# Kernel optimization log

Hardware: AMD Instinct MI355X
Metric: run time of the kernel (lower is better)

The kernel has to match this reference:

```python
import jax, jax.numpy as jnp
import numpy as np

NEG_INF = -1000000000.0

N, T, D, H = 2, 4096, 512, 8
S = D // H  # size_per_head = 64


def setup_inputs() -> dict:
    key = jax.random.key(0)
    ks = jax.random.split(key, 6)
    scale = 1.0 / np.sqrt(D)
    return {
        "query": jax.random.normal(ks[0], (N, T, D), dtype=jnp.float32),
        "reference": jax.random.normal(ks[1], (N, T, D), dtype=jnp.float32),
        "padding_mask": jnp.zeros((N, 1, 1, T), dtype=jnp.float32),
        "Wq": jax.random.normal(ks[2], (D, H, S), dtype=jnp.float32) * scale,
        "Wk": jax.random.normal(ks[3], (D, H, S), dtype=jnp.float32) * scale,
        "Wv": jax.random.normal(ks[4], (D, H, S), dtype=jnp.float32) * scale,
        "Wo": jax.random.normal(ks[5], (H, S, D), dtype=jnp.float32) * scale,
    }


def reference(query, reference, padding_mask, Wq, Wk, Wv, Wo):
    # split projections: [N,T,D] x [D,H,S] -> [N,T,H,S]
    q = jnp.einsum("NTD,DHS->NTHS", query, Wq) * (S ** -0.5)
    k = jnp.einsum("NTD,DHS->NTHS", reference, Wk)
    v = jnp.einsum("NTD,DHS->NTHS", reference, Wv)
    # scores [N,H,Q,R]; mask is 0/1, scaled by NEG_INF (as in source)
    scores = jnp.einsum("NQHS,NRHS->NHQR", q, k) + padding_mask * NEG_INF
    probs = jax.nn.softmax(scores, axis=3)
    # dropout is identity (training=False)
    ctx = jnp.einsum("NHQR,NRHS->NQHS", probs, v)
    # merge projection: [N,Q,H,S] x [H,S,D] -> [N,Q,D]
    return jnp.einsum("NTHS,HSD->NTD", ctx, Wo)
```

## Files before the change

### kernel.cpp

```cpp
#include <hip/hip_runtime.h>
#include <stdint.h>

using u16    = unsigned short;
using u32    = unsigned int;
using short8 = __attribute__((ext_vector_type(8))) short;
using s16x4  = __attribute__((ext_vector_type(4))) short;
using f32x4  = __attribute__((ext_vector_type(4))) float;
using f32x16 = __attribute__((ext_vector_type(16))) float;
using i32x4  = __attribute__((ext_vector_type(4))) int;

constexpr float LOG2E = 1.44269504088896340736f;


__device__ __forceinline__ u16 f2bf(float f) {
  uint32_t u = __builtin_bit_cast(uint32_t, f);
  return (u16)((u + 0x7fffu + ((u >> 16) & 1u)) >> 16);
}

__device__ __forceinline__ void gload16(const void* g, void* l) {
  __builtin_amdgcn_global_load_lds(
      (const __attribute__((address_space(1))) unsigned int*)g,
      (__attribute__((address_space(3))) unsigned int*)l, 16, 0, 0);
}

__device__ __forceinline__ u32 cvtpk_bf16(float lo, float hi) {
  u32 r;
  asm("v_cvt_pk_bf16_f32 %0, %1, %2" : "=v"(r) : "v"(lo), "v"(hi));
  return r;
}

__device__ __forceinline__ f32x16 zero16() {
  f32x16 z;
#pragma unroll
  for (int i = 0; i < 16; ++i) z[i] = 0.f;
  return z;
}

__device__ __forceinline__ short8 ldfrag(const u16* s, int row, int kbyte) {
  int phys = (row << 7) + (kbyte ^ ((row & 7) << 4));
  return *(const short8*)((const char*)s + phys);
}

__global__ __launch_bounds__(256) void prep_kernel(
    const float4* __restrict__ qin, const float4* __restrict__ rin,
    const float* __restrict__ mask,
    const float* __restrict__ wq, const float* __restrict__ wk,
    const float* __restrict__ wv, const float* __restrict__ wo,
    u16* __restrict__ xq, u16* __restrict__ xr,
    u16* __restrict__ wqt, u16* __restrict__ wkt,
    u16* __restrict__ wvt, u16* __restrict__ wot,
    u16* __restrict__ kfr, int* __restrict__ mflag) {
  const int gid = blockIdx.x * blockDim.x + threadIdx.x;
  const int stride = gridDim.x * blockDim.x;
  for (int i = gid; i < (2 * 4096 * 512) / 4; i += stride) {
    float4 a = qin[i], b = rin[i];
    s16x4 va = {(short)f2bf(a.x), (short)f2bf(a.y), (short)f2bf(a.z), (short)f2bf(a.w)};
    s16x4 vb = {(short)f2bf(b.x), (short)f2bf(b.y), (short)f2bf(b.z), (short)f2bf(b.w)};
    *(s16x4*)(xq + i * 4) = va;
    *(s16x4*)(xr + i * 4) = vb;
  }
  for (int i = gid; i < 512 * 512; i += stride) {
    int orow = i >> 9, ocol = i & 511;
    int si = ocol * 512 + orow;
    wqt[i] = f2bf(wq[si]);
    wkt[i] = f2bf(wk[si]);
    wvt[i] = f2bf(wv[si]);
    wot[i] = f2bf(wo[si]);
  }
  for (int i = gid; i < 16 * 4096; i += stride) {
    int head = i >> 12, key = i & 4095;
    int nn = head >> 3;
    float mv = mask[nn * 4096 + key];
    float mt = mv * (-1.0e9f * LOG2E);
    int tile = key >> 5, lqk = key & 31;
    u16* base = kfr + (((size_t)(head * 128 + tile)) * 5 + 4) * 512;
    u16* p0 = base + (size_t)lqk * 8;
    u16* p1 = base + (size_t)(32 + lqk) * 8;
    p0[0] = f2bf(mt);
#pragma unroll
    for (int j = 1; j < 8; ++j) p0[j] = 0;
#pragma unroll
    for (int j = 0; j < 8; ++j) p1[j] = 0;
    unsigned long long any = __ballot(mv != 0.0f);
    if ((threadIdx.x & 63) == 0 && any != 0ULL) atomicOr(mflag, 1);
  }
}

__device__ __forceinline__ void gemm_core(const u16* __restrict__ A, const u16* __restrict__ Bt,
                                          int K, u16* As, u16* Bs, int tm0, int tn0,
                                          f32x4 acc[4][4]) {
  const int tid = threadIdx.x;
  const int wv = tid >> 6, ln = tid & 63;
  const int lr = ln & 15, hi = ln >> 4;
  const int wr = wv >> 1, wc = wv & 1;
  const size_t rowbytes = (size_t)K * 2;
  for (int k0 = 0; k0 < K; k0 += 64) {
    __syncthreads();
    const char* Ab = (const char*)A + (size_t)tm0 * rowbytes + (size_t)k0 * 2;
    const char* Bb = (const char*)Bt + (size_t)tn0 * rowbytes + (size_t)k0 * 2;
#pragma unroll
    for (int c = 0; c < 4; ++c) {
      int lin = wv * 4096 + c * 1024 + ln * 16;
      int row = lin >> 7;
      int cb = (lin & 127) ^ ((row & 7) << 4);
      gload16(Ab + (size_t)row * rowbytes + cb, (char*)As + wv * 4096 + c * 1024);
      gload16(Bb + (size_t)row * rowbytes + cb, (char*)Bs + wv * 4096 + c * 1024);
    }
    __syncthreads();
#pragma unroll
    for (int ks = 0; ks < 2; ++ks) {
      short8 af[4], bf[4];
#pragma unroll
      for (int m = 0; m < 4; ++m) af[m] = ldfrag(As, wr * 64 + m * 16 + lr, ks * 64 + hi * 16);
#pragma unroll
      for (int n = 0; n < 4; ++n) bf[n] = ldfrag(Bs, wc * 64 + n * 16 + lr, ks * 64 + hi * 16);
#pragma unroll
      for (int m = 0; m < 4; ++m)
#pragma unroll
        for (int n = 0; n < 4; ++n)
          acc[m][n] = __builtin_amdgcn_mfma_f32_16x16x32_bf16(af[m], bf[n], acc[m][n], 0, 0, 0);
    }
  }
}

__global__ __launch_bounds__(256) void qkv_gemm(
    const u16* __restrict__ xq, const u16* __restrict__ xr,
    const u16* __restrict__ wqt, const u16* __restrict__ wkt, const u16* __restrict__ wvt,
    u16* __restrict__ qo, u16* __restrict__ kfr, u16* __restrict__ vfr) {
  __shared__ u16 As[128 * 64];
  __shared__ u16 Bs[128 * 64];
  const int z = blockIdx.z;
  const u16* A  = (z == 0) ? xq : xr;
  const u16* Bt = (z == 0) ? wqt : (z == 1) ? wkt : wvt;
  const int tm0 = blockIdx.x * 128, tn0 = blockIdx.y * 128;
  f32x4 acc[4][4];
#pragma unroll
  for (int m = 0; m < 4; ++m)
#pragma unroll
    for (int n = 0; n < 4; ++n) { f32x4 zz = {0.f, 0.f, 0.f, 0.f}; acc[m][n] = zz; }
  gemm_core(A, Bt, 512, As, Bs, tm0, tn0, acc);

  const int tid = threadIdx.x, wv = tid >> 6, ln = tid & 63, lr = ln & 15, hi = ln >> 4;
  const int wr = wv >> 1, wc = wv & 1;
  const float scale = (z == 0) ? 0.125f * LOG2E : 1.0f;
#pragma unroll
  for (int m = 0; m < 4; ++m) {
#pragma unroll
    for (int n = 0; n < 4; ++n) {
#pragma unroll
      for (int r = 0; r < 4; ++r) {
        int rg = tm0 + wr * 64 + m * 16 + hi * 4 + r;
        int cg = tn0 + wc * 64 + n * 16 + lr;
        int nb = rg >> 12, t = rg & 4095;
        int h = cg >> 6, s = cg & 63;
        int head = nb * 8 + h;
        u16 b = f2bf(acc[m][n][r] * scale);
        if (z == 0) {
          qo[((size_t)head * 4096 + t) * 64 + s] = b;
        } else if (z == 1) {
          int tile = t >> 5, lqk = t & 31;
          int ks = s >> 4, hh = (s >> 3) & 1, j = s & 7;
          kfr[((((size_t)(head * 128 + tile)) * 5 + ks) * 64 + hh * 32 + lqk) * 8 + j] = b;
        } else {
          int tile = t >> 5, w5 = t & 31;
          int ks = w5 >> 4, hh = (w5 >> 3) & 1, j = w5 & 7;
          int st = s >> 5, lqs = s & 31;
          vfr[((((size_t)(head * 128 + tile)) * 4 + ks * 2 + st) * 64 + hh * 32 + lqs) * 8 + j] = b;
        }
      }
    }
  }
}

__global__ __launch_bounds__(512, 2) void attn14_kernel(
    const u16* __restrict__ q, const char* __restrict__ kfr, const char* __restrict__ vfr,
    u16* __restrict__ ctx, const int* __restrict__ mflag) {
  __shared__ float cmb[4][32][64];
  __shared__ float cl[4][64];
  const int id = blockIdx.x;
  const int xcd = id & 7, slot = id >> 3;
  const int head = xcd * 2 + (slot >> 4);
  const int qb = slot & 15;
  const int n = head >> 3, h = head & 7;
  const int tid = threadIdx.x, wv = tid >> 6, ln = tid & 63;
  const int lq = ln & 31, hi = ln >> 5, hi4 = hi * 4;
  const int qt = wv & 3, kg = wv >> 2;
  const int q0 = qb * 256 + qt * 64;
  const bool aug = (*mflag != 0);

  short8 qfa[5], qfb[5];
  {
    const char* qp = (const char*)(q + (size_t)head * 4096 * 64) + (size_t)(q0 + lq) * 128 + hi * 16;
#pragma unroll
    for (int ks = 0; ks < 4; ++ks) {
      qfa[ks] = *(const short8*)(qp + ks * 32);
      qfb[ks] = *(const short8*)(qp + 32 * 128 + ks * 32);
    }
    short8 z = {0, 0, 0, 0, 0, 0, 0, 0};
    if (hi == 0) z[0] = (short)0x3F80;
    qfa[4] = z;
    qfb[4] = z;
  }

  const char* kp = kfr + (size_t)head * 655360 + (size_t)(kg * 64) * 5120 + ln * 16;
  const char* vp = vfr + (size_t)head * 524288 + (size_t)(kg * 64) * 4096 + ln * 16;

  short8 kA[5];
#pragma unroll
  for (int s = 0; s < 4; ++s) kA[s] = *(const short8*)(kp + s * 1024);
  if (aug) kA[4] = *(const short8*)(kp + 4 * 1024);
  kp += 5120;

  f32x16 cacc0a = zero16(), cacc1a = zero16();
  f32x16 cacc0b = zero16(), cacc1b = zero16();
  f32x16 la = zero16(), lb = zero16();

  for (int it = 0; it < 64; ++it) {
    short8 vA[4];
#pragma unroll
    for (int s = 0; s < 4; ++s) vA[s] = *(const short8*)(vp + s * 1024);
    vp += 4096;

    f32x16 Sa = zero16(), Sb = zero16();
    __builtin_amdgcn_s_setprio(1);
#pragma unroll
    for (int ks = 0; ks < 4; ++ks) {
      Sa = __builtin_amdgcn_mfma_f32_32x32x16_bf16(kA[ks], qfa[ks], Sa, 0, 0, 0);
      Sb = __builtin_amdgcn_mfma_f32_32x32x16_bf16(kA[ks], qfb[ks], Sb, 0, 0, 0);
    }
    if (aug) {
      Sa = __builtin_amdgcn_mfma_f32_32x32x16_bf16(kA[4], qfa[4], Sa, 0, 0, 0);
      Sb = __builtin_amdgcn_mfma_f32_32x32x16_bf16(kA[4], qfb[4], Sb, 0, 0, 0);
    }
    __builtin_amdgcn_s_setprio(0);

    short8 kN[5];
#pragma unroll
    for (int s = 0; s < 4; ++s) kN[s] = *(const short8*)(kp + s * 1024);
    if (aug) kN[4] = *(const short8*)(kp + 4 * 1024);
    kp += 5120;

    float pa_[16], pb_[16];
#pragma unroll
    for (int r = 0; r < 16; ++r) { pa_[r] = __builtin_amdgcn_exp2f(Sa[r]); la[r] += pa_[r]; }
#pragma unroll
    for (int r = 0; r < 16; ++r) { pb_[r] = __builtin_amdgcn_exp2f(Sb[r]); lb[r] += pb_[r]; }

    short8 pa0, pa1, pb0, pb1;
#define SHF32(x) ((u32)__shfl_xor((int)(x), 32))
#define MKFRAGS(P, FA, FB)                                                          \
    {                                                                               \
      u32 A01 = cvtpk_bf16(P[0], P[1]), B23 = cvtpk_bf16(P[2], P[3]);               \
      u32 C45 = cvtpk_bf16(P[4], P[5]), D67 = cvtpk_bf16(P[6], P[7]);               \
      u32 E89 = cvtpk_bf16(P[8], P[9]), F01 = cvtpk_bf16(P[10], P[11]);             \
      u32 G23 = cvtpk_bf16(P[12], P[13]), H45 = cvtpk_bf16(P[14], P[15]);           \
      u32 A01x = SHF32(A01), B23x = SHF32(B23), C45x = SHF32(C45), D67x = SHF32(D67);\
      u32 E89x = SHF32(E89), F01x = SHF32(F01), G23x = SHF32(G23), H45x = SHF32(H45);\
      i32x4 fa = {(int)(hi ? C45x : A01), (int)(hi ? D67x : B23),                   \
                  (int)(hi ? C45 : A01x), (int)(hi ? D67 : B23x)};                  \
      i32x4 fb = {(int)(hi ? G23x : E89), (int)(hi ? H45x : F01),                   \
                  (int)(hi ? G23 : E89x), (int)(hi ? H45 : F01x)};                  \
      FA = __builtin_bit_cast(short8, fa);                                          \
      FB = __builtin_bit_cast(short8, fb);                                          \
    }
    MKFRAGS(pa_, pa0, pa1);
    MKFRAGS(pb_, pb0, pb1);
#undef MKFRAGS
#undef SHF32

    __builtin_amdgcn_s_setprio(1);
    cacc0a = __builtin_amdgcn_mfma_f32_32x32x16_bf16(pa0, vA[0], cacc0a, 0, 0, 0);
    cacc1a = __builtin_amdgcn_mfma_f32_32x32x16_bf16(pa0, vA[1], cacc1a, 0, 0, 0);
    cacc0b = __builtin_amdgcn_mfma_f32_32x32x16_bf16(pb0, vA[0], cacc0b, 0, 0, 0);
    cacc1b = __builtin_amdgcn_mfma_f32_32x32x16_bf16(pb0, vA[1], cacc1b, 0, 0, 0);
    cacc0a = __builtin_amdgcn_mfma_f32_32x32x16_bf16(pa1, vA[2], cacc0a, 0, 0, 0);
    cacc1a = __builtin_amdgcn_mfma_f32_32x32x16_bf16(pa1, vA[3], cacc1a, 0, 0, 0);
    cacc0b = __builtin_amdgcn_mfma_f32_32x32x16_bf16(pb1, vA[2], cacc0b, 0, 0, 0);
    cacc1b = __builtin_amdgcn_mfma_f32_32x32x16_bf16(pb1, vA[3], cacc1b, 0, 0, 0);
    __builtin_amdgcn_s_setprio(0);

#pragma unroll
    for (int s = 0; s < 4; ++s) kA[s] = kN[s];
    if (aug) kA[4] = kN[4];
  }

  float lra, lrb;
  {
    float ta[16], tb[16];
#pragma unroll
    for (int r = 0; r < 16; ++r) { ta[r] = la[r]; tb[r] = lb[r]; }
#pragma unroll
    for (int d = 8; d > 0; d >>= 1)
#pragma unroll
      for (int r = 0; r < d; ++r) { ta[r] += ta[r + d]; tb[r] += tb[r + d]; }
    lra = ta[0] + __shfl_xor(ta[0], 32);
    lrb = tb[0] + __shfl_xor(tb[0], 32);
  }

  u16* cp = ctx + (size_t)(n * 4096 + q0) * 512 + h * 64;
  if (kg == 1) {
#pragma unroll
    for (int r = 0; r < 16; ++r) {
      cmb[qt][r][ln] = cacc0a[r];
      cmb[qt][r + 16][ln] = cacc1a[r];
    }
    cl[qt][ln] = lra;
  }
  __syncthreads();
  if (kg == 0) {
#pragma unroll
    for (int r = 0; r < 16; ++r) {
      cacc0a[r] += cmb[qt][r][ln];
      cacc1a[r] += cmb[qt][r + 16][ln];
    }
    lra += cl[qt][ln];
    float li = 1.0f / lra;
    int lii = __builtin_bit_cast(int, li);
#pragma unroll
    for (int r = 0; r < 16; ++r) {
      int cr = (r & 3) + ((r >> 2) << 3) + hi4;
      float inv = __builtin_bit_cast(float, __builtin_amdgcn_ds_bpermute(cr << 2, lii));
      cp[(size_t)cr * 512 + lq] = f2bf(cacc0a[r] * inv);
      cp[(size_t)cr * 512 + 32 + lq] = f2bf(cacc1a[r] * inv);
    }
  }
  __syncthreads();
  if (kg == 1) {
#pragma unroll
    for (int r = 0; r < 16; ++r) {
      cmb[qt][r][ln] = cacc0b[r];
      cmb[qt][r + 16][ln] = cacc1b[r];
    }
    cl[qt][ln] = lrb;
  }
  __syncthreads();
  if (kg == 0) {
#pragma unroll
    for (int r = 0; r < 16; ++r) {
      cacc0b[r] += cmb[qt][r][ln];
      cacc1b[r] += cmb[qt][r + 16][ln];
    }
    lrb += cl[qt][ln];
    float li = 1.0f / lrb;
    int lii = __builtin_bit_cast(int, li);
    u16* cpb = cp + (size_t)32 * 512;
#pragma unroll
    for (int r = 0; r < 16; ++r) {
      int cr = (r & 3) + ((r >> 2) << 3) + hi4;
      float inv = __builtin_bit_cast(float, __builtin_amdgcn_ds_bpermute(cr << 2, lii));
      cpb[(size_t)cr * 512 + lq] = f2bf(cacc0b[r] * inv);
      cpb[(size_t)cr * 512 + 32 + lq] = f2bf(cacc1b[r] * inv);
    }
  }
}

__global__ __launch_bounds__(256) void out_gemm(
    const u16* __restrict__ ctx, const u16* __restrict__ wot, float* __restrict__ out) {
  __shared__ u16 As[128 * 64];
  __shared__ u16 Bs[128 * 64];
  const int tm0 = blockIdx.x * 128, tn0 = blockIdx.y * 128;
  f32x4 acc[4][4];
#pragma unroll
  for (int m = 0; m < 4; ++m)
#pragma unroll
    for (int n = 0; n < 4; ++n) { f32x4 zz = {0.f, 0.f, 0.f, 0.f}; acc[m][n] = zz; }
  gemm_core(ctx, wot, 512, As, Bs, tm0, tn0, acc);

  const int tid = threadIdx.x, wv = tid >> 6, ln = tid & 63, lr = ln & 15, hi = ln >> 4;
  const int wr = wv >> 1, wc = wv & 1;
#pragma unroll
  for (int m = 0; m < 4; ++m)
#pragma unroll
    for (int n = 0; n < 4; ++n)
#pragma unroll
      for (int r = 0; r < 4; ++r) {
        int rg = tm0 + wr * 64 + m * 16 + hi * 4 + r;
        int cg = tn0 + wc * 64 + n * 16 + lr;
        out[(size_t)rg * 512 + cg] = acc[m][n][r];
      }
}

extern "C" void kernel_launch(void* const* d_in, const int* in_sizes, int n_in,
                              void* d_out, int out_size, void* d_ws, size_t ws_size,
                              hipStream_t stream) {
  (void)in_sizes; (void)n_in; (void)out_size; (void)ws_size;
  const float* qin  = (const float*)d_in[0];
  const float* rin  = (const float*)d_in[1];
  const float* mask = (const float*)d_in[2];
  const float* wq   = (const float*)d_in[3];
  const float* wk   = (const float*)d_in[4];
  const float* wv   = (const float*)d_in[5];
  const float* wo   = (const float*)d_in[6];

  char* ws = (char*)d_ws;
  u16* xq   = (u16*)(ws + 0);
  u16* ctx  = (u16*)(ws + 0);
  u16* xr   = (u16*)(ws + 8388608);
  u16* wqt  = (u16*)(ws + 16777216);
  u16* wkt  = (u16*)(ws + 17301504);
  u16* wvt  = (u16*)(ws + 17825792);
  u16* wot  = (u16*)(ws + 18350080);
  u16* qo   = (u16*)(ws + 18874368);
  u16* kfr  = (u16*)(ws + 27262976);
  u16* vfr  = (u16*)(ws + 37748736);
  int* mflag = (int*)(ws + 46137344);

  hipMemsetAsync(mflag, 0, 4, stream);
  prep_kernel<<<2048, 256, 0, stream>>>((const float4*)qin, (const float4*)rin, mask,
                                        wq, wk, wv, wo, xq, xr, wqt, wkt, wvt, wot,
                                        kfr, mflag);
  qkv_gemm<<<dim3(64, 4, 3), 256, 0, stream>>>(xq, xr, wqt, wkt, wvt, qo, kfr, vfr);
  attn14_kernel<<<256, 512, 0, stream>>>(qo, (const char*)kfr, (const char*)vfr, ctx, mflag);
  out_gemm<<<dim3(64, 4), 256, 0, stream>>>(ctx, wot, (float*)d_out);
}
```

Measured before the change: 137.2 us.

## Transpose PV MFMA to drop P shuffles and stage ctx via LDS

The V fragment layout written by the QKV GEMM is permuted so the PV product can be computed as V^T·P with the operands swapped. The exp'd scores can then feed the MFMA directly as packed bf16 without cross-lane shuffles. The epilogue now writes normalized context through a padded LDS tile and lets both wave groups emit coalesced row stores, replacing scattered 2-byte stores and bpermutes. This adds more __syncthreads and LDS traffic in the epilogue.

```diff
diff --git a/kernel.cpp b/kernel.cpp
--- a/kernel.cpp
+++ b/kernel.cpp
@@ -162,21 +162,25 @@
           int ks = s >> 4, hh = (s >> 3) & 1, j = s & 7;
           kfr[((((size_t)(head * 128 + tile)) * 5 + ks) * 64 + hh * 32 + lqk) * 8 + j] = b;
         } else {
-          int tile = t >> 5, w5 = t & 31;
-          int ks = w5 >> 4, hh = (w5 >> 3) & 1, j = w5 & 7;
+          int tile = t >> 5, key5 = t & 31;
+          int c = key5 >> 4, w = key5 & 15;
+          int hh2 = (w >> 2) & 1;
+          int j2 = (w & 3) + ((w >> 3) << 2);
           int st = s >> 5, lqs = s & 31;
-          vfr[((((size_t)(head * 128 + tile)) * 4 + ks * 2 + st) * 64 + hh * 32 + lqs) * 8 + j] = b;
+          vfr[((((size_t)(head * 128 + tile)) * 4 + c * 2 + st) * 64 + hh2 * 32 + lqs) * 8 + j2] = b;
         }
       }
     }
   }
 }
 
-__global__ __launch_bounds__(512, 2) void attn14_kernel(
+__global__ __launch_bounds__(512, 2) void attn15_kernel(
     const u16* __restrict__ q, const char* __restrict__ kfr, const char* __restrict__ vfr,
     u16* __restrict__ ctx, const int* __restrict__ mflag) {
-  __shared__ float cmb[4][32][64];
+  __shared__ __align__(16) char smem[4 * 32 * 65 * 4];
   __shared__ float cl[4][64];
+  float (*cmbraw)[32][64] = (float(*)[32][64])smem;
+  float (*cmb2)[32][65]   = (float(*)[32][65])smem;
   const int id = blockIdx.x;
   const int xcd = id & 7, slot = id >> 3;
   const int head = xcd * 2 + (slot >> 4);
@@ -216,9 +220,9 @@
   f32x16 la = zero16(), lb = zero16();
 
   for (int it = 0; it < 64; ++it) {
-    short8 vA[4];
-#pragma unroll
-    for (int s = 0; s < 4; ++s) vA[s] = *(const short8*)(vp + s * 1024);
+    short8 vt[4];
+#pragma unroll
+    for (int s = 0; s < 4; ++s) vt[s] = *(const short8*)(vp + s * 1024);
     vp += 4096;
 
     f32x16 Sa = zero16(), Sb = zero16();
@@ -246,37 +250,31 @@
 #pragma unroll
     for (int r = 0; r < 16; ++r) { pb_[r] = __builtin_amdgcn_exp2f(Sb[r]); lb[r] += pb_[r]; }
 
-    short8 pa0, pa1, pb0, pb1;
-#define SHF32(x) ((u32)__shfl_xor((int)(x), 32))
-#define MKFRAGS(P, FA, FB)                                                          \
-    {                                                                               \
-      u32 A01 = cvtpk_bf16(P[0], P[1]), B23 = cvtpk_bf16(P[2], P[3]);               \
-      u32 C45 = cvtpk_bf16(P[4], P[5]), D67 = cvtpk_bf16(P[6], P[7]);               \
-      u32 E89 = cvtpk_bf16(P[8], P[9]), F01 = cvtpk_bf16(P[10], P[11]);             \
-      u32 G23 = cvtpk_bf16(P[12], P[13]), H45 = cvtpk_bf16(P[14], P[15]);           \
-      u32 A01x = SHF32(A01), B23x = SHF32(B23), C45x = SHF32(C45), D67x = SHF32(D67);\
-      u32 E89x = SHF32(E89), F01x = SHF32(F01), G23x = SHF32(G23), H45x = SHF32(H45);\
-      i32x4 fa = {(int)(hi ? C45x : A01), (int)(hi ? D67x : B23),                   \
-                  (int)(hi ? C45 : A01x), (int)(hi ? D67 : B23x)};                  \
-      i32x4 fb = {(int)(hi ? G23x : E89), (int)(hi ? H45x : F01),                   \
-                  (int)(hi ? G23 : E89x), (int)(hi ? H45 : F01x)};                  \
-      FA = __builtin_bit_cast(short8, fa);                                          \
-      FB = __builtin_bit_cast(short8, fb);                                          \
-    }
-    MKFRAGS(pa_, pa0, pa1);
-    MKFRAGS(pb_, pb0, pb1);
-#undef MKFRAGS
-#undef SHF32
+    short8 pA0, pA1, pB0, pB1;
+    {
+      i32x4 f0 = {(int)cvtpk_bf16(pa_[0], pa_[1]), (int)cvtpk_bf16(pa_[2], pa_[3]),
+                  (int)cvtpk_bf16(pa_[4], pa_[5]), (int)cvtpk_bf16(pa_[6], pa_[7])};
+      i32x4 f1 = {(int)cvtpk_bf16(pa_[8], pa_[9]), (int)cvtpk_bf16(pa_[10], pa_[11]),
+                  (int)cvtpk_bf16(pa_[12], pa_[13]), (int)cvtpk_bf16(pa_[14], pa_[15])};
+      i32x4 g0 = {(int)cvtpk_bf16(pb_[0], pb_[1]), (int)cvtpk_bf16(pb_[2], pb_[3]),
+                  (int)cvtpk_bf16(pb_[4], pb_[5]), (int)cvtpk_bf16(pb_[6], pb_[7])};
+      i32x4 g1 = {(int)cvtpk_bf16(pb_[8], pb_[9]), (int)cvtpk_bf16(pb_[10], pb_[11]),
+                  (int)cvtpk_bf16(pb_[12], pb_[13]), (int)cvtpk_bf16(pb_[14], pb_[15])};
+      pA0 = __builtin_bit_cast(short8, f0);
+      pA1 = __builtin_bit_cast(short8, f1);
+      pB0 = __builtin_bit_cast(short8, g0);
+      pB1 = __builtin_bit_cast(short8, g1);
+    }
 
     __builtin_amdgcn_s_setprio(1);
-    cacc0a = __builtin_amdgcn_mfma_f32_32x32x16_bf16(pa0, vA[0], cacc0a, 0, 0, 0);
-    cacc1a = __builtin_amdgcn_mfma_f32_32x32x16_bf16(pa0, vA[1], cacc1a, 0, 0, 0);
-    cacc0b = __builtin_amdgcn_mfma_f32_32x32x16_bf16(pb0, vA[0], cacc0b, 0, 0, 0);
-    cacc1b = __builtin_amdgcn_mfma_f32_32x32x16_bf16(pb0, vA[1], cacc1b, 0, 0, 0);
-    cacc0a = __builtin_amdgcn_mfma_f32_32x32x16_bf16(pa1, vA[2], cacc0a, 0, 0, 0);
-    cacc1a = __builtin_amdgcn_mfma_f32_32x32x16_bf16(pa1, vA[3], cacc1a, 0, 0, 0);
-    cacc0b = __builtin_amdgcn_mfma_f32_32x32x16_bf16(pb1, vA[2], cacc0b, 0, 0, 0);
-    cacc1b = __builtin_amdgcn_mfma_f32_32x32x16_bf16(pb1, vA[3], cacc1b, 0, 0, 0);
+    cacc0a = __builtin_amdgcn_mfma_f32_32x32x16_bf16(vt[0], pA0, cacc0a, 0, 0, 0);
+    cacc1a = __builtin_amdgcn_mfma_f32_32x32x16_bf16(vt[1], pA0, cacc1a, 0, 0, 0);
+    cacc0b = __builtin_amdgcn_mfma_f32_32x32x16_bf16(vt[0], pB0, cacc0b, 0, 0, 0);
+    cacc1b = __builtin_amdgcn_mfma_f32_32x32x16_bf16(vt[1], pB0, cacc1b, 0, 0, 0);
+    cacc0a = __builtin_amdgcn_mfma_f32_32x32x16_bf16(vt[2], pA1, cacc0a, 0, 0, 0);
+    cacc1a = __builtin_amdgcn_mfma_f32_32x32x16_bf16(vt[3], pA1, cacc1a, 0, 0, 0);
+    cacc0b = __builtin_amdgcn_mfma_f32_32x32x16_bf16(vt[2], pB1, cacc0b, 0, 0, 0);
+    cacc1b = __builtin_amdgcn_mfma_f32_32x32x16_bf16(vt[3], pB1, cacc1b, 0, 0, 0);
     __builtin_amdgcn_s_setprio(0);
 
 #pragma unroll
@@ -297,61 +295,47 @@
     lrb = tb[0] + __shfl_xor(tb[0], 32);
   }
 
-  u16* cp = ctx + (size_t)(n * 4096 + q0) * 512 + h * 64;
-  if (kg == 1) {
-#pragma unroll
-    for (int r = 0; r < 16; ++r) {
-      cmb[qt][r][ln] = cacc0a[r];
-      cmb[qt][r + 16][ln] = cacc1a[r];
-    }
-    cl[qt][ln] = lra;
-  }
-  __syncthreads();
-  if (kg == 0) {
-#pragma unroll
-    for (int r = 0; r < 16; ++r) {
-      cacc0a[r] += cmb[qt][r][ln];
-      cacc1a[r] += cmb[qt][r + 16][ln];
-    }
-    lra += cl[qt][ln];
-    float li = 1.0f / lra;
-    int lii = __builtin_bit_cast(int, li);
-#pragma unroll
-    for (int r = 0; r < 16; ++r) {
-      int cr = (r & 3) + ((r >> 2) << 3) + hi4;
-      float inv = __builtin_bit_cast(float, __builtin_amdgcn_ds_bpermute(cr << 2, lii));
-      cp[(size_t)cr * 512 + lq] = f2bf(cacc0a[r] * inv);
-      cp[(size_t)cr * 512 + 32 + lq] = f2bf(cacc1a[r] * inv);
-    }
-  }
-  __syncthreads();
-  if (kg == 1) {
-#pragma unroll
-    for (int r = 0; r < 16; ++r) {
-      cmb[qt][r][ln] = cacc0b[r];
-      cmb[qt][r + 16][ln] = cacc1b[r];
-    }
-    cl[qt][ln] = lrb;
-  }
-  __syncthreads();
-  if (kg == 0) {
-#pragma unroll
-    for (int r = 0; r < 16; ++r) {
-      cacc0b[r] += cmb[qt][r][ln];
-      cacc1b[r] += cmb[qt][r + 16][ln];
-    }
-    lrb += cl[qt][ln];
-    float li = 1.0f / lrb;
-    int lii = __builtin_bit_cast(int, li);
-    u16* cpb = cp + (size_t)32 * 512;
-#pragma unroll
-    for (int r = 0; r < 16; ++r) {
-      int cr = (r & 3) + ((r >> 2) << 3) + hi4;
-      float inv = __builtin_bit_cast(float, __builtin_amdgcn_ds_bpermute(cr << 2, lii));
-      cpb[(size_t)cr * 512 + lq] = f2bf(cacc0b[r] * inv);
-      cpb[(size_t)cr * 512 + 32 + lq] = f2bf(cacc1b[r] * inv);
-    }
-  }
+  auto epilogue = [&](f32x16& c0, f32x16& c1, float lr, int qofs) {
+    if (kg == 1) {
+#pragma unroll
+      for (int r = 0; r < 16; ++r) {
+        cmbraw[qt][r][ln] = c0[r];
+        cmbraw[qt][r + 16][ln] = c1[r];
+      }
+      cl[qt][ln] = lr;
+    }
+    __syncthreads();
+    if (kg == 0) {
+#pragma unroll
+      for (int r = 0; r < 16; ++r) {
+        c0[r] += cmbraw[qt][r][ln];
+        c1[r] += cmbraw[qt][r + 16][ln];
+      }
+      lr += cl[qt][ln];
+    }
+    __syncthreads();
+    if (kg == 0) {
+      float li = 1.0f / lr;
+#pragma unroll
+      for (int r = 0; r < 16; ++r) {
+        int s0 = (r & 3) + ((r >> 2) << 3) + hi4;
+        cmb2[qt][lq][s0] = c0[r] * li;
+        cmb2[qt][lq][32 + s0] = c1[r] * li;
+      }
+    }
+    __syncthreads();
+    {
+      u16* cpx = ctx + (size_t)(n * 4096 + qb * 256 + qt * 64 + qofs) * 512 + h * 64;
+#pragma unroll
+      for (int rr = 0; rr < 16; ++rr) {
+        int qq = kg * 16 + rr;
+        cpx[(size_t)qq * 512 + ln] = f2bf(cmb2[qt][qq][ln]);
+      }
+    }
+    __syncthreads();
+  };
+  epilogue(cacc0a, cacc1a, lra, 0);
+  epilogue(cacc0b, cacc1b, lrb, 32);
 }
 
 __global__ __launch_bounds__(256) void out_gemm(
@@ -410,6 +394,6 @@
                                         wq, wk, wv, wo, xq, xr, wqt, wkt, wvt, wot,
                                         kfr, mflag);
   qkv_gemm<<<dim3(64, 4, 3), 256, 0, stream>>>(xq, xr, wqt, wkt, wvt, qo, kfr, vfr);
-  attn14_kernel<<<256, 512, 0, stream>>>(qo, (const char*)kfr, (const char*)vfr, ctx, mflag);
+  attn15_kernel<<<256, 512, 0, stream>>>(qo, (const char*)kfr, (const char*)vfr, ctx, mflag);
   out_gemm<<<dim3(64, 4), 256, 0, stream>>>(ctx, wot, (float*)d_out);
 }
```

New measurement: 127.6 us. 1.08x faster.
